# Optimization experiments

Hardware: AMD Instinct MI355X
Metric: run time of the kernel (lower is better)

Reference implementation:

```python
import jax, jax.numpy as jnp
import numpy as np


def setup_inputs() -> dict:
    key = jax.random.key(0)
    k1, k2 = jax.random.split(key)
    B, C, F = 8192, 10000, 2048
    x = jax.random.normal(k1, (B, F), dtype=jnp.float32)
    means = jax.random.normal(k2, (C, F), dtype=jnp.float32)
    return {"x": x, "means": means}


def reference(x, means):
    # Negative squared Euclidean distance from each sample to each class mean.
    # Same math as sum((x[:,None,:]-means[None,:,:])**2, -1), expressed via the
    x_sq = jnp.sum(x * x, axis=-1, keepdims=True)          # [B, 1]
    m_sq = jnp.sum(means * means, axis=-1)                  # [C]
    cross = jnp.einsum("bf,cf->bc", x, means)              # [B, C] GEMM
    dist_sq = x_sq + m_sq[None, :] - 2.0 * cross            # [B, C]
    return -dist_sq
```

## Files before the change

kernel.cpp:

```cpp
#include <hip/hip_runtime.h>
#include <hip/hip_bf16.h>
#include <stdint.h>

#define BDIM 8192
#define CDIM 10000
#define CPAD 10240
#define FDIM 2048

#define BM 256
#define BN 256
#define BKB 64
#define NT (FDIM / BKB)
#define NI (NT / 2)
#define TM (BDIM / BM)
#define TN (CPAD / BN)
#define NWG (TM * TN)

#define HT_BYTES   8192
#define DBUF_BYTES 32768
#define EPI_WAVE_BYTES 4352
#define LDS_BYTES  65536

#define QSF   (6.5f / 127.0f)
#define INVQ  (127.0f / 6.5f)
#define TSC   (2.0f * QSF * QSF)

typedef __attribute__((ext_vector_type(4))) int   i32x4;
typedef __attribute__((ext_vector_type(4))) float f32x4;

#define AS1 __attribute__((address_space(1)))
#define AS3 __attribute__((address_space(3)))

__global__ __launch_bounds__(256) void convert_rows(
    const float* __restrict__ xsrc, const float* __restrict__ msrc,
    signed char* __restrict__ Xq, signed char* __restrict__ Mq,
    float* __restrict__ xsq, float* __restrict__ msq)
{
    const int b = blockIdx.x;
    const int tid = threadIdx.x;

    const float* src;
    signed char* drow;
    float* sq;
    int row;
    if (b < BDIM) {
        row = b; src = xsrc + (size_t)row * FDIM;
        drow = Xq + (size_t)row * FDIM; sq = xsq + row;
    } else {
        row = b - BDIM;
        drow = Mq + (size_t)row * FDIM; sq = msq + row;
        if (row >= CDIM) {
            ((uint2*)drow)[tid] = make_uint2(0, 0);
            if (tid == 0) *sq = 0.0f;
            return;
        }
        src = msrc + (size_t)row * FDIM;
    }

    const float4* s = (const float4*)src;
    float4 v0 = s[tid * 2 + 0];
    float4 v1 = s[tid * 2 + 1];

    float f[8] = {v0.x, v0.y, v0.z, v0.w, v1.x, v1.y, v1.z, v1.w};
    float ssum = 0.0f;
    union { unsigned char u[8]; uint2 v; } pk;
#pragma unroll
    for (int j = 0; j < 8; ++j) {
        ssum += f[j] * f[j];
        int q = (int)__builtin_rintf(f[j] * INVQ);
        q = q > 127 ? 127 : (q < -127 ? -127 : q);
        pk.u[j] = (unsigned char)(q & 0xff);
    }
    ((uint2*)drow)[tid] = pk.v;

#pragma unroll
    for (int off = 32; off > 0; off >>= 1)
        ssum += __shfl_down(ssum, off, 64);
    __shared__ float red[4];
    if ((tid & 63) == 0) red[tid >> 6] = ssum;
    __syncthreads();
    if (tid == 0) *sq = red[0] + red[1] + red[2] + red[3];
}

#define MIDSYNC() do { \
    __builtin_amdgcn_s_barrier(); \
    asm volatile("s_waitcnt lgkmcnt(0)" ::: "memory"); \
    __builtin_amdgcn_sched_barrier(0); \
} while (0)

#define ENDBAR() do { \
    __builtin_amdgcn_s_barrier(); \
    __builtin_amdgcn_sched_barrier(0); \
} while (0)

#define SCHEDBAR() __builtin_amdgcn_sched_barrier(0)

#define QUAD16(MH, AV, BV) do { \
    __builtin_amdgcn_s_setprio(1); \
    _Pragma("unroll") \
    for (int nh = 0; nh < 2; ++nh) \
      _Pragma("unroll") \
      for (int f = 0; f < 4; ++f) \
        _Pragma("unroll") \
        for (int f2 = 0; f2 < 2; ++f2) \
          acc[(MH)*4+f][nh*2+f2] = __builtin_amdgcn_mfma_i32_16x16x64_i8( \
              AV[f], BV[nh][f2], acc[(MH)*4+f][nh*2+f2], 0, 0, 0); \
    __builtin_amdgcn_s_setprio(0); \
} while (0)

__global__ __launch_bounds__(512, 2) void nscm_gemm(
    const signed char* __restrict__ Xq, const signed char* __restrict__ Mq,
    const float* __restrict__ xsq, const float* __restrict__ msq,
    float* __restrict__ out)
{
    extern __shared__ char lds[];

    const int tid  = threadIdx.x;
    const int lane = tid & 63;
    const int wave = tid >> 6;
    const int wr = wave >> 2;
    const int wc = wave & 3;
    const int fr = lane & 15;
    const int kq = lane >> 4;

    const int bid = blockIdx.x;
    const int xcd = bid & 7;
    const int c   = bid >> 3;
    const int sub = c >> 5;
    const int tile_m = xcd * 4 + (c & 3);
    const int tile_n = sub * 8 + ((c >> 2) & 7);
    const int row0 = tile_m * BM;
    const int col0 = tile_n * BN;

    const int sw  = tid >> 2;
    const int sce = (((tid & 3) ^ ((tid >> 3) & 3))) * 16;
    const int rslot = (kq ^ ((fr >> 1) & 3)) * 16;

    i32x4 acc[8][4] = {};
    i32x4 avA[4], avB[4], bv0[2][2], bv1[2][2];

    auto stageA = [&](int kt, int buf, int h) {
        const int grow = row0 + (sw >> 6) * 128 + h * 64 + (sw & 63);
        const signed char* src = Xq + (size_t)grow * FDIM + kt * BKB + sce;
        char* dst = lds + buf * DBUF_BYTES + h * HT_BYTES + wave * 1024;
        __builtin_amdgcn_global_load_lds((const AS1 void*)src,
                                         (AS3 void*)dst, 16, 0, 0);
    };
    auto stageB = [&](int kt, int buf, int h) {
        const int grow = col0 + (sw >> 5) * 64 + h * 32 + (sw & 31);
        const signed char* src = Mq + (size_t)grow * FDIM + kt * BKB + sce;
        char* dst = lds + buf * DBUF_BYTES + 16384 + h * HT_BYTES + wave * 1024;
        __builtin_amdgcn_global_load_lds((const AS1 void*)src,
                                         (AS3 void*)dst, 16, 0, 0);
    };

    auto loadA = [&](int buf, int mh, i32x4 (&dst)[4]) {
        const char* base = lds + buf * DBUF_BYTES + mh * HT_BYTES;
#pragma unroll
        for (int f = 0; f < 4; ++f) {
            const int w = wr * 64 + f * 16 + fr;
            dst[f] = *(const i32x4*)(base + w * 64 + rslot);
        }
    };
    auto loadB = [&](int buf, int nh, i32x4 (&dst)[2]) {
        const char* base = lds + buf * DBUF_BYTES + 16384 + nh * HT_BYTES;
#pragma unroll
        for (int f = 0; f < 2; ++f) {
            const int w = wc * 32 + f * 16 + fr;
            dst[f] = *(const i32x4*)(base + w * 64 + rslot);
        }
    };

    stageA(0, 0, 0); stageB(0, 0, 0); stageA(0, 0, 1); stageB(0, 0, 1);
    stageA(1, 1, 0); stageB(1, 1, 0);
    asm volatile("s_waitcnt vmcnt(2)" ::: "memory");
    __builtin_amdgcn_s_barrier();
    SCHEDBAR();
    loadA(0, 0, avA); loadB(0, 0, bv0[0]); loadB(0, 1, bv0[1]);
    SCHEDBAR();

    for (int t = 0; t < NI; ++t) {
        const int kO1 = 2 * t + 1;
        const int kE2 = (2 * t + 2) & (NT - 1);
        const int kO3 = (2 * t + 3) & (NT - 1);

        stageA(kO1, 1, 1);
        stageB(kO1, 1, 1);
        MIDSYNC();
        loadA(0, 1, avB);
        SCHEDBAR();
        QUAD16(0, avA, bv0);
        ENDBAR();

        stageA(kE2, 0, 0);
        stageB(kE2, 0, 0);
        asm volatile("s_waitcnt vmcnt(2)" ::: "memory");
        MIDSYNC();
        loadA(1, 0, avA); loadB(1, 0, bv1[0]); loadB(1, 1, bv1[1]);
        SCHEDBAR();
        QUAD16(1, avB, bv0);
        ENDBAR();

        stageA(kE2, 0, 1);
        stageB(kE2, 0, 1);
        MIDSYNC();
        loadA(1, 1, avB);
        SCHEDBAR();
        QUAD16(0, avA, bv1);
        ENDBAR();

        stageA(kO3, 1, 0);
        stageB(kO3, 1, 0);
        asm volatile("s_waitcnt vmcnt(2)" ::: "memory");
        MIDSYNC();
        loadA(0, 0, avA); loadB(0, 0, bv0[0]); loadB(0, 1, bv0[1]);
        SCHEDBAR();
        QUAD16(1, avB, bv1);
        ENDBAR();
    }

    asm volatile("s_waitcnt vmcnt(0) lgkmcnt(0)" ::: "memory");
    __builtin_amdgcn_s_barrier();
    SCHEDBAR();

    float* wtile = (float*)(lds + wave * EPI_WAVE_BYTES);
    const int rr = lane >> 4;
    const int cq = lane & 15;
    const int gc = col0 + wc * 64 + cq * 4;
    float ms0 = 0.f, ms1 = 0.f, ms2 = 0.f, ms3 = 0.f;
    if (gc < CDIM) {
        ms0 = msq[gc]; ms1 = msq[gc + 1]; ms2 = msq[gc + 2]; ms3 = msq[gc + 3];
    }

#pragma unroll
    for (int p = 0; p < 8; ++p) {
#pragma unroll
        for (int fn = 0; fn < 4; ++fn) {
            const int lr = kq * 4;
            const int lc = fn * 16 + fr;
#pragma unroll
            for (int r = 0; r < 4; ++r)
                wtile[(lr + r) * 68 + lc] = (float)acc[p][fn][r];
        }
        asm volatile("s_waitcnt lgkmcnt(0)" ::: "memory");
        SCHEDBAR();

        if (gc < CDIM) {
#pragma unroll
            for (int i = 0; i < 4; ++i) {
                const int row = i * 4 + rr;
                f32x4 v = *(const f32x4*)&wtile[row * 68 + cq * 4];
                const int gr = row0 + wr * 128 + p * 16 + row;
                const float xsv = xsq[gr];
                f32x4 o;
                o[0] = TSC * v[0] - xsv - ms0;
                o[1] = TSC * v[1] - xsv - ms1;
                o[2] = TSC * v[2] - xsv - ms2;
                o[3] = TSC * v[3] - xsv - ms3;
                __builtin_nontemporal_store(
                    o, (f32x4*)(out + (size_t)gr * CDIM + gc));
            }
        }
        asm volatile("s_waitcnt lgkmcnt(0)" ::: "memory");
        SCHEDBAR();
    }
}

extern "C" void kernel_launch(void* const* d_in, const int* in_sizes, int n_in,
                              void* d_out, int out_size, void* d_ws, size_t ws_size,
                              hipStream_t stream) {
    const float* x     = (const float*)d_in[0];
    const float* means = (const float*)d_in[1];
    float* out = (float*)d_out;

    char* ws = (char*)d_ws;
    signed char* Xq = (signed char*)ws;
    signed char* Mq = (signed char*)(ws + (size_t)BDIM * FDIM);
    float* xsq = (float*)(ws + (size_t)BDIM * FDIM + (size_t)CPAD * FDIM);
    float* msq = xsq + BDIM;

    (void)hipFuncSetAttribute((const void*)nscm_gemm,
                              hipFuncAttributeMaxDynamicSharedMemorySize,
                              LDS_BYTES);

    convert_rows<<<BDIM + CPAD, 256, 0, stream>>>(x, means, Xq, Mq, xsq, msq);

    nscm_gemm<<<NWG, 512, LDS_BYTES, stream>>>(Xq, Mq, xsq, msq, out);
}
```

Measured before the change: 223.1 us.

## Load B operand directly from global into registers, stage only A in LDS

The main loop is restructured so only the X tile goes through LDS (double-buffered, 2x16KB), while each wave loads its slice of the means tile straight from global memory into registers one k-step ahead. The four-phase half-tile schedule becomes a simpler two-phase loop with one full 8x4 MFMA block per k-step. LDS use drops from 64KB to about 34KB. In exchange, each B row is fetched redundantly by the two waves that share a column slice, and the direct global loads are not swizzled, so they may coalesce worse and the latency is exposed to registers.

```diff
diff --git a/kernel.cpp b/kernel.cpp
--- a/kernel.cpp
+++ b/kernel.cpp
@@ -11,15 +11,13 @@
 #define BN 256
 #define BKB 64
 #define NT (FDIM / BKB)
-#define NI (NT / 2)
 #define TM (BDIM / BM)
 #define TN (CPAD / BN)
 #define NWG (TM * TN)
 
-#define HT_BYTES   8192
-#define DBUF_BYTES 32768
+#define ABUF_BYTES 16384
 #define EPI_WAVE_BYTES 4352
-#define LDS_BYTES  65536
+#define LDS_BYTES  34816
 
 #define QSF   (6.5f / 127.0f)
 #define INVQ  (127.0f / 6.5f)
@@ -82,30 +80,27 @@
     if (tid == 0) *sq = red[0] + red[1] + red[2] + red[3];
 }
 
-#define MIDSYNC() do { \
+#define SCHEDBAR() __builtin_amdgcn_sched_barrier(0)
+
+#define ITER(T, BUF, BVC, BVN) do { \
+    loadA(BUF); \
+    asm volatile("s_waitcnt lgkmcnt(0)" ::: "memory"); \
     __builtin_amdgcn_s_barrier(); \
-    asm volatile("s_waitcnt lgkmcnt(0)" ::: "memory"); \
-    __builtin_amdgcn_sched_barrier(0); \
-} while (0)
-
-#define ENDBAR() do { \
+    SCHEDBAR(); \
+    stageA(((T) + 2) & (NT - 1), BUF); \
+    loadBdir(((T) + 1) & (NT - 1), BVN); \
+    asm volatile("s_waitcnt vmcnt(6)" ::: "memory"); \
     __builtin_amdgcn_s_barrier(); \
-    __builtin_amdgcn_sched_barrier(0); \
-} while (0)
-
-#define SCHEDBAR() __builtin_amdgcn_sched_barrier(0)
-
-#define QUAD16(MH, AV, BV) do { \
+    SCHEDBAR(); \
     __builtin_amdgcn_s_setprio(1); \
     _Pragma("unroll") \
-    for (int nh = 0; nh < 2; ++nh) \
+    for (int f = 0; f < 8; ++f) \
       _Pragma("unroll") \
-      for (int f = 0; f < 4; ++f) \
-        _Pragma("unroll") \
-        for (int f2 = 0; f2 < 2; ++f2) \
-          acc[(MH)*4+f][nh*2+f2] = __builtin_amdgcn_mfma_i32_16x16x64_i8( \
-              AV[f], BV[nh][f2], acc[(MH)*4+f][nh*2+f2], 0, 0, 0); \
+      for (int j = 0; j < 4; ++j) \
+        acc[f][j] = __builtin_amdgcn_mfma_i32_16x16x64_i8( \
+            av[f], BVC[j], acc[f][j], 0, 0, 0); \
     __builtin_amdgcn_s_setprio(0); \
+    SCHEDBAR(); \
 } while (0)
 
 __global__ __launch_bounds__(512, 2) void nscm_gemm(
@@ -137,86 +132,45 @@
     const int rslot = (kq ^ ((fr >> 1) & 3)) * 16;
 
     i32x4 acc[8][4] = {};
-    i32x4 avA[4], avB[4], bv0[2][2], bv1[2][2];
-
-    auto stageA = [&](int kt, int buf, int h) {
-        const int grow = row0 + (sw >> 6) * 128 + h * 64 + (sw & 63);
-        const signed char* src = Xq + (size_t)grow * FDIM + kt * BKB + sce;
-        char* dst = lds + buf * DBUF_BYTES + h * HT_BYTES + wave * 1024;
-        __builtin_amdgcn_global_load_lds((const AS1 void*)src,
-                                         (AS3 void*)dst, 16, 0, 0);
+    i32x4 av[8], bvA[4], bvB[4];
+
+    auto stageA = [&](int kt, int buf) {
+#pragma unroll
+        for (int l = 0; l < 2; ++l) {
+            const int grow = row0 + l * 128 + sw;
+            const signed char* src = Xq + (size_t)grow * FDIM + kt * BKB + sce;
+            char* dst = lds + buf * ABUF_BYTES + l * 8192 + wave * 1024;
+            __builtin_amdgcn_global_load_lds((const AS1 void*)src,
+                                             (AS3 void*)dst, 16, 0, 0);
+        }
     };
-    auto stageB = [&](int kt, int buf, int h) {
-        const int grow = col0 + (sw >> 5) * 64 + h * 32 + (sw & 31);
-        const signed char* src = Mq + (size_t)grow * FDIM + kt * BKB + sce;
-        char* dst = lds + buf * DBUF_BYTES + 16384 + h * HT_BYTES + wave * 1024;
-        __builtin_amdgcn_global_load_lds((const AS1 void*)src,
-                                         (AS3 void*)dst, 16, 0, 0);
+
+    auto loadA = [&](int buf) {
+        const char* base = lds + buf * ABUF_BYTES;
+#pragma unroll
+        for (int f = 0; f < 8; ++f) {
+            const int ri = wr * 128 + f * 16 + fr;
+            av[f] = *(const i32x4*)(base + ri * 64 + rslot);
+        }
     };
 
-    auto loadA = [&](int buf, int mh, i32x4 (&dst)[4]) {
-        const char* base = lds + buf * DBUF_BYTES + mh * HT_BYTES;
-#pragma unroll
-        for (int f = 0; f < 4; ++f) {
-            const int w = wr * 64 + f * 16 + fr;
-            dst[f] = *(const i32x4*)(base + w * 64 + rslot);
+    auto loadBdir = [&](int kt, i32x4 (&dst)[4]) {
+#pragma unroll
+        for (int j = 0; j < 4; ++j) {
+            const int w = col0 + wc * 64 + j * 16 + fr;
+            dst[j] = *(const i32x4*)(Mq + (size_t)w * FDIM + kt * BKB + kq * 16);
         }
     };
-    auto loadB = [&](int buf, int nh, i32x4 (&dst)[2]) {
-        const char* base = lds + buf * DBUF_BYTES + 16384 + nh * HT_BYTES;
-#pragma unroll
-        for (int f = 0; f < 2; ++f) {
-            const int w = wc * 32 + f * 16 + fr;
-            dst[f] = *(const i32x4*)(base + w * 64 + rslot);
-        }
-    };
-
-    stageA(0, 0, 0); stageB(0, 0, 0); stageA(0, 0, 1); stageB(0, 0, 1);
-    stageA(1, 1, 0); stageB(1, 1, 0);
-    asm volatile("s_waitcnt vmcnt(2)" ::: "memory");
+
+    stageA(0, 0); stageA(1, 1);
+    loadBdir(0, bvA);
+    asm volatile("s_waitcnt vmcnt(6)" ::: "memory");
     __builtin_amdgcn_s_barrier();
     SCHEDBAR();
-    loadA(0, 0, avA); loadB(0, 0, bv0[0]); loadB(0, 1, bv0[1]);
-    SCHEDBAR();
-
-    for (int t = 0; t < NI; ++t) {
-        const int kO1 = 2 * t + 1;
-        const int kE2 = (2 * t + 2) & (NT - 1);
-        const int kO3 = (2 * t + 3) & (NT - 1);
-
-        stageA(kO1, 1, 1);
-        stageB(kO1, 1, 1);
-        MIDSYNC();
-        loadA(0, 1, avB);
-        SCHEDBAR();
-        QUAD16(0, avA, bv0);
-        ENDBAR();
-
-        stageA(kE2, 0, 0);
-        stageB(kE2, 0, 0);
-        asm volatile("s_waitcnt vmcnt(2)" ::: "memory");
-        MIDSYNC();
-        loadA(1, 0, avA); loadB(1, 0, bv1[0]); loadB(1, 1, bv1[1]);
-        SCHEDBAR();
-        QUAD16(1, avB, bv0);
-        ENDBAR();
-
-        stageA(kE2, 0, 1);
-        stageB(kE2, 0, 1);
-        MIDSYNC();
-        loadA(1, 1, avB);
-        SCHEDBAR();
-        QUAD16(0, avA, bv1);
-        ENDBAR();
-
-        stageA(kO3, 1, 0);
-        stageB(kO3, 1, 0);
-        asm volatile("s_waitcnt vmcnt(2)" ::: "memory");
-        MIDSYNC();
-        loadA(0, 0, avA); loadB(0, 0, bv0[0]); loadB(0, 1, bv0[1]);
-        SCHEDBAR();
-        QUAD16(1, avB, bv1);
-        ENDBAR();
+
+    for (int t = 0; t < NT; t += 2) {
+        ITER(t,     0, bvA, bvB);
+        ITER(t + 1, 1, bvB, bvA);
     }
 
     asm volatile("s_waitcnt vmcnt(0) lgkmcnt(0)" ::: "memory");
```

Result: slower. 306.2 us (+37.3%).
